# Kernel optimization log

Hardware: AMD Instinct MI355X
Metric: run time of the kernel (lower is better)

The kernel has to match this reference:

```python
import jax, jax.numpy as jnp
import numpy as np

NUM_EMBEDDINGS = 512
EMBEDDING_DIM = 64


def setup_inputs() -> dict:
    key = jax.random.key(0)
    k1, k2 = jax.random.split(key)
    # latent from (identity) encoder, channels-last so view(-1, D) is valid
    z = jax.random.normal(k1, (32, 64, 64, EMBEDDING_DIM), dtype=jnp.float32)
    # codebook init: uniform(-1/K, 1/K) as in the torch module
    scale = 1.0 / NUM_EMBEDDINGS
    codebook = jax.random.uniform(
        k2, (NUM_EMBEDDINGS, EMBEDDING_DIM), dtype=jnp.float32,
        minval=-scale, maxval=scale)
    return {"z": z, "codebook": codebook}


def reference(z, codebook):
    # encoder = identity
    B, H, W, D = z.shape
    zf = z.reshape(-1, D)                                   # [N, D]
    # squared L2 distances: ||z||^2 + ||e||^2 - 2 z.e
    d = (jnp.sum(zf * zf, axis=1, keepdims=True)
         + jnp.sum(codebook * codebook, axis=1)
         - 2.0 * jnp.matmul(zf, codebook.T))                # [N, K]
    idx = jnp.argmin(d, axis=1)                             # [N]
    z_quantized = codebook[idx].reshape(z.shape)            # gather + reshape
    # decoder = identity
    x_recon = z_quantized
    return (x_recon, z_quantized)
```

## Files before the change

### kernel.cpp

```cpp
#include <hip/hip_runtime.h>
#include <math.h>

#define K_CODES 512
#define DIM 64
#define ROWS_PER_BLOCK 128
#define MROWS 128

__device__ __forceinline__ float np_pairwise_sumsq(const float* v) {
#pragma clang fp contract(off)
    float p[DIM];
#pragma unroll
    for (int j = 0; j < DIM; ++j) p[j] = v[j] * v[j];
    float r[8];
#pragma unroll
    for (int a = 0; a < 8; ++a) r[a] = p[a];
#pragma unroll
    for (int i = 8; i < DIM; i += 8) {
#pragma unroll
        for (int a = 0; a < 8; ++a) r[a] = r[a] + p[i + a];
    }
    return ((r[0] + r[1]) + (r[2] + r[3])) + ((r[4] + r[5]) + (r[6] + r[7]));
}

__device__ __forceinline__ float np_dot8acc(const float* zr, const float* ck) {
#pragma clang fp contract(off)
    float a0 = 0.f, a1 = 0.f, a2 = 0.f, a3 = 0.f;
    float a4 = 0.f, a5 = 0.f, a6 = 0.f, a7 = 0.f;
#pragma unroll
    for (int j = 0; j < DIM; j += 8) {
        a0 = fmaf(zr[j + 0], ck[j + 0], a0);
        a1 = fmaf(zr[j + 1], ck[j + 1], a1);
        a2 = fmaf(zr[j + 2], ck[j + 2], a2);
        a3 = fmaf(zr[j + 3], ck[j + 3], a3);
        a4 = fmaf(zr[j + 4], ck[j + 4], a4);
        a5 = fmaf(zr[j + 5], ck[j + 5], a5);
        a6 = fmaf(zr[j + 6], ck[j + 6], a6);
        a7 = fmaf(zr[j + 7], ck[j + 7], a7);
    }
    return ((a0 + a1) + (a2 + a3)) + ((a4 + a5) + (a6 + a7));
}

__global__ __launch_bounds__(256, 4) void vq_argmin_gather(
    const float* __restrict__ z, const float* __restrict__ cb,
    float* __restrict__ out, int n_rows) {
#pragma clang fp contract(off)
    __shared__ float esq_lds[K_CODES];
    __shared__ float red_d[ROWS_PER_BLOCK];
    __shared__ int   red_b[ROWS_PER_BLOCK];
    __shared__ int   best_lds[ROWS_PER_BLOCK];

    const int t = threadIdx.x;
    const int tr  = t & (ROWS_PER_BLOCK - 1);
    const int row = blockIdx.x * ROWS_PER_BLOCK + tr;
    const int k0 = __builtin_amdgcn_readfirstlane((t >> 7) << 8);

    float zr[DIM];
    const float4* zp = (const float4*)(z + (size_t)row * DIM);
#pragma unroll
    for (int j = 0; j < DIM / 4; ++j) {
        float4 v = zp[j];
        zr[4 * j + 0] = v.x; zr[4 * j + 1] = v.y;
        zr[4 * j + 2] = v.z; zr[4 * j + 3] = v.w;
    }
#pragma unroll
    for (int j = 0; j < DIM; ++j) { asm volatile("" : "+v"(zr[j])); }

    for (int c = t; c < K_CODES; c += 256)
        esq_lds[c] = np_pairwise_sumsq(cb + (size_t)c * DIM);
    __syncthreads();

    const float zsq = np_pairwise_sumsq(zr);
    float dmin = INFINITY;
    int best = k0;
    const float* __restrict__ cbase = cb + (size_t)k0 * DIM;
#pragma unroll 2
    for (int kk = 0; kk < K_CODES / 2; ++kk) {
        const float dot = np_dot8acc(zr, cbase + (size_t)kk * DIM);
        const float tkv = zsq + esq_lds[k0 + kk];
        const float m = 2.0f * dot;
        const float d = tkv - m;
        if (d < dmin) { dmin = d; best = k0 + kk; }
    }
    if (t >= ROWS_PER_BLOCK) { red_d[tr] = dmin; red_b[tr] = best; }
    __syncthreads();
    if (t < ROWS_PER_BLOCK) {
        int b = (red_d[tr] < dmin) ? red_b[tr] : best;
        best_lds[tr] = b;
    }
    __syncthreads();

    const float4* cb4 = (const float4*)cb;
    float4* o = (float4*)out;
    const size_t out1_off = (size_t)n_rows * (DIM / 4);
    const size_t grow = (size_t)blockIdx.x * ROWS_PER_BLOCK * (DIM / 4);
#pragma unroll
    for (int i = t; i < ROWS_PER_BLOCK * (DIM / 4); i += 256) {
        const int r = i >> 4;
        const int j = i & 15;
        const float4 v = cb4[(size_t)best_lds[r] * (DIM / 4) + j];
        const size_t g = grow + (size_t)r * (DIM / 4) + j;
        o[g] = v;
        o[g + out1_off] = v;
    }
}

typedef __bf16 bfx8 __attribute__((ext_vector_type(8)));
typedef float  f32x4 __attribute__((ext_vector_type(4)));

#define EPS_GAP 3.0e-5f

__device__ __forceinline__ void split_bf16(float x, unsigned short& h, unsigned short& l) {
    unsigned int xb = __float_as_uint(x);
    unsigned int hb = (xb + 0x8000u) & 0xffff0000u;
    h = (unsigned short)(hb >> 16);
    float lf = x - __uint_as_float(hb);
    l = (unsigned short)((__float_as_uint(lf) + 0x8000u) >> 16);
}

__global__ void vq_prep(const float* __restrict__ cb,
                        unsigned short* __restrict__ wh,
                        unsigned short* __restrict__ wl,
                        float* __restrict__ esq,
                        int* __restrict__ gcnt) {
    const int id = blockIdx.x * 256 + threadIdx.x;
    if (id == 0) gcnt[0] = 0;
    const int l = id & 63;
    const int s = (id >> 6) & 1;
    const int t = id >> 7;
    const int code = t * 16 + (l & 15);
    const int d0 = s * 32 + (l >> 4) * 8;
    const float* p = cb + (size_t)code * DIM + d0;
    float4 v0 = *(const float4*)p;
    float4 v1 = *(const float4*)(p + 4);
    float f[8] = {v0.x, v0.y, v0.z, v0.w, v1.x, v1.y, v1.z, v1.w};
    union { unsigned short u[8]; uint4 q; } H, L;
#pragma unroll
    for (int j = 0; j < 8; ++j) split_bf16(f[j], H.u[j], L.u[j]);
    *(uint4*)(wh + (size_t)id * 8) = H.q;
    *(uint4*)(wl + (size_t)id * 8) = L.q;
    if (id < K_CODES) esq[id] = np_pairwise_sumsq(cb + (size_t)id * DIM);
}

__global__ __launch_bounds__(512)
__attribute__((amdgpu_waves_per_eu(1, 2))) void vq_mfma_main(
    const float* __restrict__ z,
    const unsigned short* __restrict__ wfrag,
    const float* __restrict__ esq_g,
    const float* __restrict__ cb,
    float* __restrict__ out,
    int* __restrict__ gcnt, int* __restrict__ grows,
    int n_rows) {
    __shared__ unsigned short b_lds[K_CODES * DIM * 2];
    __shared__ float esq_lds[K_CODES];
    __shared__ int   best_lds[MROWS];

    const int t = threadIdx.x;
    const int wave = t >> 6;
    const int lane = t & 63;
    const int lg = lane >> 4;
    const int lr = lane & 15;
    const int rb = blockIdx.x * MROWS;
    const int wrb = rb + wave * 16;

    {
        const uint4* src = (const uint4*)wfrag;
        uint4* dst = (uint4*)b_lds;
#pragma unroll
        for (int i = 0; i < 16; ++i) dst[t + i * 512] = src[t + i * 512];
    }
    if (t < K_CODES) esq_lds[t] = esq_g[t];

    bfx8 a_hi[2], a_lo[2];
#pragma unroll
    for (int s = 0; s < 2; ++s) {
        const float* zp = z + (size_t)(wrb + lr) * DIM + s * 32 + lg * 8;
        float4 v0 = *(const float4*)zp;
        float4 v1 = *(const float4*)(zp + 4);
        float f[8] = {v0.x, v0.y, v0.z, v0.w, v1.x, v1.y, v1.z, v1.w};
        union { unsigned short u[8]; bfx8 b; } H, L;
#pragma unroll
        for (int j = 0; j < 8; ++j) split_bf16(f[j], H.u[j], L.u[j]);
        a_hi[s] = H.b;
        a_lo[s] = L.b;
    }
    __syncthreads();

    float b1[4], b2[4];
    int   k1[4];
#pragma unroll
    for (int i = 0; i < 4; ++i) { b1[i] = INFINITY; b2[i] = INFINITY; k1[i] = 0; }

    for (int tt = 0; tt < 32; ++tt) {
        const int s0 = ((tt * 2 + 0) * 64 + lane) * 8;
        const int s1 = ((tt * 2 + 1) * 64 + lane) * 8;
        bfx8 bh0 = *(const bfx8*)(b_lds + s0);
        bfx8 bh1 = *(const bfx8*)(b_lds + s1);
        bfx8 bl0 = *(const bfx8*)(b_lds + 32768 + s0);
        bfx8 bl1 = *(const bfx8*)(b_lds + 32768 + s1);

        f32x4 acc = {0.f, 0.f, 0.f, 0.f};
        acc = __builtin_amdgcn_mfma_f32_16x16x32_bf16(a_hi[0], bh0, acc, 0, 0, 0);
        acc = __builtin_amdgcn_mfma_f32_16x16x32_bf16(a_hi[1], bh1, acc, 0, 0, 0);
        acc = __builtin_amdgcn_mfma_f32_16x16x32_bf16(a_hi[0], bl0, acc, 0, 0, 0);
        acc = __builtin_amdgcn_mfma_f32_16x16x32_bf16(a_hi[1], bl1, acc, 0, 0, 0);
        acc = __builtin_amdgcn_mfma_f32_16x16x32_bf16(a_lo[0], bh0, acc, 0, 0, 0);
        acc = __builtin_amdgcn_mfma_f32_16x16x32_bf16(a_lo[1], bh1, acc, 0, 0, 0);

        const float ev = esq_lds[tt * 16 + lr];
        const int   kk = tt * 16 + lr;
#pragma unroll
        for (int i = 0; i < 4; ++i) {
            float s = fmaf(-2.0f, acc[i], ev);
            b2[i] = fminf(fmaxf(s, b1[i]), b2[i]);
            bool c = s < b1[i];
            b1[i] = c ? s : b1[i];
            k1[i] = c ? kk : k1[i];
        }
    }

#pragma unroll
    for (int m = 1; m <= 8; m <<= 1) {
#pragma unroll
        for (int i = 0; i < 4; ++i) {
            float ob1 = __shfl_xor(b1[i], m);
            int   ok1 = __shfl_xor(k1[i], m);
            float ob2 = __shfl_xor(b2[i], m);
            float nb2 = fminf(fmaxf(b1[i], ob1), fminf(b2[i], ob2));
            bool take = (ob1 < b1[i]) || (ob1 == b1[i] && ok1 < k1[i]);
            b1[i] = take ? ob1 : b1[i];
            k1[i] = take ? ok1 : k1[i];
            b2[i] = nb2;
        }
    }

    if (lr == 0) {
#pragma unroll
        for (int i = 0; i < 4; ++i) {
            const int rl = wave * 16 + lg * 4 + i;
            best_lds[rl] = k1[i];
            if (b2[i] - b1[i] <= EPS_GAP) {
                int p = atomicAdd(gcnt, 1);
                grows[p] = rb + rl;
            }
        }
    }
    __syncthreads();

    const float4* cb4 = (const float4*)cb;
    float4* o = (float4*)out;
    const size_t out1_off = (size_t)n_rows * (DIM / 4);
    const size_t grow = (size_t)blockIdx.x * MROWS * (DIM / 4);
#pragma unroll
    for (int i = t; i < MROWS * (DIM / 4); i += 512) {
        const int r = i >> 4;
        const int j = i & 15;
        const float4 v = cb4[(size_t)best_lds[r] * (DIM / 4) + j];
        const size_t g = grow + (size_t)r * (DIM / 4) + j;
        o[g] = v;
        o[g + out1_off] = v;
    }
}

__global__ __launch_bounds__(256, 1) void vq_fixup(
    const float* __restrict__ z, const float* __restrict__ cb,
    const float* __restrict__ esq_g,
    const int* __restrict__ gcnt, const int* __restrict__ grows,
    float* __restrict__ out, int n_rows) {
#pragma clang fp contract(off)
    const int lane = threadIdx.x & 63;
    const int wid = (blockIdx.x * 256 + threadIdx.x) >> 6;
    const int nf = gcnt[0];

    for (int fi = wid; fi < nf; fi += 1024) {
        const int row = __builtin_amdgcn_readfirstlane(grows[fi]);
        const float* zp = z + (size_t)row * DIM;
        float zs[DIM];
#pragma unroll
        for (int j = 0; j < DIM; ++j) zs[j] = zp[j];

        const float zsq = np_pairwise_sumsq(zs);
        float dmin = INFINITY;
        int bk = lane * 8;
        const float* cbase = cb + (size_t)(lane * 8) * DIM;
#pragma unroll
        for (int c = 0; c < 8; ++c) {
            const float dot = np_dot8acc(zs, cbase + (size_t)c * DIM);
            const float tkv = zsq + esq_g[lane * 8 + c];
            const float m2 = 2.0f * dot;
            const float d = tkv - m2;
            if (d < dmin) { dmin = d; bk = lane * 8 + c; }
        }
#pragma unroll
        for (int m = 1; m <= 32; m <<= 1) {
            float od = __shfl_xor(dmin, m);
            int   ob = __shfl_xor(bk, m);
            bool take = (od < dmin) || (od == dmin && ob < bk);
            dmin = take ? od : dmin;
            bk = take ? ob : bk;
        }
        if (lane < 16) {
            const float4 v = ((const float4*)cb)[(size_t)bk * (DIM / 4) + lane];
            float4* o = (float4*)out;
            const size_t g = (size_t)row * (DIM / 4) + lane;
            o[g] = v;
            o[g + (size_t)n_rows * (DIM / 4)] = v;
        }
    }
}

extern "C" void kernel_launch(void* const* d_in, const int* in_sizes, int n_in,
                              void* d_out, int out_size, void* d_ws, size_t ws_size,
                              hipStream_t stream) {
    const float* z  = (const float*)d_in[0];
    const float* cb = (const float*)d_in[1];
    float* out = (float*)d_out;

    const int n_rows = in_sizes[0] / DIM;

    const size_t frag_elems = (size_t)K_CODES * DIM;
    const size_t WS_NEED = frag_elems * 2 * 2 + K_CODES * 4 + 16 + (size_t)n_rows * 4;
    if (ws_size >= WS_NEED && (n_rows % MROWS) == 0) {
        unsigned short* wh = (unsigned short*)d_ws;
        unsigned short* wl = wh + frag_elems;
        float* esq = (float*)(wl + frag_elems);
        int* gcnt  = (int*)(esq + K_CODES);
        int* grows = gcnt + 4;
        vq_prep<<<dim3(16), dim3(256), 0, stream>>>(cb, wh, wl, esq, gcnt);
        vq_mfma_main<<<dim3(n_rows / MROWS), dim3(512), 0, stream>>>(
            z, wh, esq, cb, out, gcnt, grows, n_rows);
        vq_fixup<<<dim3(256), dim3(256), 0, stream>>>(
            z, cb, esq, gcnt, grows, out, n_rows);
    } else {
        vq_argmin_gather<<<dim3(n_rows / ROWS_PER_BLOCK), dim3(256), 0, stream>>>(
            z, cb, out, n_rows);
    }
}
```

Baseline: 167.6 us.

## Switch to 32x32x16 MFMA tiles and process 512 rows per block

Replaces the 16x16x32 bf16 MFMA tiling with 32x32x16 tiles, so each wave handles 32 rows against 32 codes per step. It also re-lays out the codebook fragments in the prep kernel to match. Each block now covers 512 rows in two sequential groups, amortising the 128KB LDS codebook load over four times as many rows. The aim is fewer LDS reads per FLOP and less per-block staging overhead. The costs are a larger register footprint (16 accumulators plus 16 running best/second-best/index values), more shuffle reduction steps, and only 256 blocks, which may reduce occupancy and tail balance.

```diff
diff --git a/kernel.cpp b/kernel.cpp
--- a/kernel.cpp
+++ b/kernel.cpp
@@ -4,7 +4,8 @@
 #define K_CODES 512
 #define DIM 64
 #define ROWS_PER_BLOCK 128
-#define MROWS 128
+#define BROWS 512
+#define GROUPS 2
 
 __device__ __forceinline__ float np_pairwise_sumsq(const float* v) {
 #pragma clang fp contract(off)
@@ -105,7 +106,7 @@
 }
 
 typedef __bf16 bfx8 __attribute__((ext_vector_type(8)));
-typedef float  f32x4 __attribute__((ext_vector_type(4)));
+typedef float  f32x16 __attribute__((ext_vector_type(16)));
 
 #define EPS_GAP 3.0e-5f
 
@@ -125,10 +126,10 @@
     const int id = blockIdx.x * 256 + threadIdx.x;
     if (id == 0) gcnt[0] = 0;
     const int l = id & 63;
-    const int s = (id >> 6) & 1;
-    const int t = id >> 7;
-    const int code = t * 16 + (l & 15);
-    const int d0 = s * 32 + (l >> 4) * 8;
+    const int kk = (id >> 6) & 3;
+    const int tile = id >> 8;
+    const int code = tile * 32 + (l & 31);
+    const int d0 = kk * 16 + (l >> 5) * 8;
     const float* p = cb + (size_t)code * DIM + d0;
     float4 v0 = *(const float4*)p;
     float4 v1 = *(const float4*)(p + 4);
@@ -152,15 +153,14 @@
     int n_rows) {
     __shared__ unsigned short b_lds[K_CODES * DIM * 2];
     __shared__ float esq_lds[K_CODES];
-    __shared__ int   best_lds[MROWS];
+    __shared__ int   best_lds[BROWS];
 
     const int t = threadIdx.x;
     const int wave = t >> 6;
     const int lane = t & 63;
-    const int lg = lane >> 4;
-    const int lr = lane & 15;
-    const int rb = blockIdx.x * MROWS;
-    const int wrb = rb + wave * 16;
+    const int lc = lane & 31;
+    const int lh = lane >> 5;
+    const int rb = blockIdx.x * BROWS;
 
     {
         const uint4* src = (const uint4*)wfrag;
@@ -169,78 +169,88 @@
         for (int i = 0; i < 16; ++i) dst[t + i * 512] = src[t + i * 512];
     }
     if (t < K_CODES) esq_lds[t] = esq_g[t];
-
-    bfx8 a_hi[2], a_lo[2];
-#pragma unroll
-    for (int s = 0; s < 2; ++s) {
-        const float* zp = z + (size_t)(wrb + lr) * DIM + s * 32 + lg * 8;
-        float4 v0 = *(const float4*)zp;
-        float4 v1 = *(const float4*)(zp + 4);
-        float f[8] = {v0.x, v0.y, v0.z, v0.w, v1.x, v1.y, v1.z, v1.w};
-        union { unsigned short u[8]; bfx8 b; } H, L;
-#pragma unroll
-        for (int j = 0; j < 8; ++j) split_bf16(f[j], H.u[j], L.u[j]);
-        a_hi[s] = H.b;
-        a_lo[s] = L.b;
-    }
-    __syncthreads();
-
-    float b1[4], b2[4];
-    int   k1[4];
-#pragma unroll
-    for (int i = 0; i < 4; ++i) { b1[i] = INFINITY; b2[i] = INFINITY; k1[i] = 0; }
-
-    for (int tt = 0; tt < 32; ++tt) {
-        const int s0 = ((tt * 2 + 0) * 64 + lane) * 8;
-        const int s1 = ((tt * 2 + 1) * 64 + lane) * 8;
-        bfx8 bh0 = *(const bfx8*)(b_lds + s0);
-        bfx8 bh1 = *(const bfx8*)(b_lds + s1);
-        bfx8 bl0 = *(const bfx8*)(b_lds + 32768 + s0);
-        bfx8 bl1 = *(const bfx8*)(b_lds + 32768 + s1);
-
-        f32x4 acc = {0.f, 0.f, 0.f, 0.f};
-        acc = __builtin_amdgcn_mfma_f32_16x16x32_bf16(a_hi[0], bh0, acc, 0, 0, 0);
-        acc = __builtin_amdgcn_mfma_f32_16x16x32_bf16(a_hi[1], bh1, acc, 0, 0, 0);
-        acc = __builtin_amdgcn_mfma_f32_16x16x32_bf16(a_hi[0], bl0, acc, 0, 0, 0);
-        acc = __builtin_amdgcn_mfma_f32_16x16x32_bf16(a_hi[1], bl1, acc, 0, 0, 0);
-        acc = __builtin_amdgcn_mfma_f32_16x16x32_bf16(a_lo[0], bh0, acc, 0, 0, 0);
-        acc = __builtin_amdgcn_mfma_f32_16x16x32_bf16(a_lo[1], bh1, acc, 0, 0, 0);
-
-        const float ev = esq_lds[tt * 16 + lr];
-        const int   kk = tt * 16 + lr;
-#pragma unroll
-        for (int i = 0; i < 4; ++i) {
-            float s = fmaf(-2.0f, acc[i], ev);
-            b2[i] = fminf(fmaxf(s, b1[i]), b2[i]);
-            bool c = s < b1[i];
-            b1[i] = c ? s : b1[i];
-            k1[i] = c ? kk : k1[i];
-        }
-    }
-
-#pragma unroll
-    for (int m = 1; m <= 8; m <<= 1) {
-#pragma unroll
-        for (int i = 0; i < 4; ++i) {
-            float ob1 = __shfl_xor(b1[i], m);
-            int   ok1 = __shfl_xor(k1[i], m);
-            float ob2 = __shfl_xor(b2[i], m);
-            float nb2 = fminf(fmaxf(b1[i], ob1), fminf(b2[i], ob2));
-            bool take = (ob1 < b1[i]) || (ob1 == b1[i] && ok1 < k1[i]);
-            b1[i] = take ? ob1 : b1[i];
-            k1[i] = take ? ok1 : k1[i];
-            b2[i] = nb2;
-        }
-    }
-
-    if (lr == 0) {
-#pragma unroll
-        for (int i = 0; i < 4; ++i) {
-            const int rl = wave * 16 + lg * 4 + i;
-            best_lds[rl] = k1[i];
-            if (b2[i] - b1[i] <= EPS_GAP) {
-                int p = atomicAdd(gcnt, 1);
-                grows[p] = rb + rl;
+    __syncthreads();
+
+#pragma unroll 1
+    for (int g = 0; g < GROUPS; ++g) {
+        const int grb = rb + g * (BROWS / GROUPS) + wave * 32;
+
+        bfx8 a_hi[4], a_lo[4];
+#pragma unroll
+        for (int kk = 0; kk < 4; ++kk) {
+            const float* zp = z + (size_t)(grb + lc) * DIM + kk * 16 + lh * 8;
+            float4 v0 = *(const float4*)zp;
+            float4 v1 = *(const float4*)(zp + 4);
+            float f[8] = {v0.x, v0.y, v0.z, v0.w, v1.x, v1.y, v1.z, v1.w};
+            union { unsigned short u[8]; bfx8 b; } H, L;
+#pragma unroll
+            for (int j = 0; j < 8; ++j) split_bf16(f[j], H.u[j], L.u[j]);
+            a_hi[kk] = H.b;
+            a_lo[kk] = L.b;
+        }
+
+        float b1[16], b2[16];
+        int   k1[16];
+#pragma unroll
+        for (int i = 0; i < 16; ++i) { b1[i] = INFINITY; b2[i] = INFINITY; k1[i] = 0; }
+
+        for (int tt = 0; tt < 16; ++tt) {
+            bfx8 bh[4], bl[4];
+#pragma unroll
+            for (int kk = 0; kk < 4; ++kk) {
+                const int s = ((tt * 4 + kk) * 64 + lane) * 8;
+                bh[kk] = *(const bfx8*)(b_lds + s);
+                bl[kk] = *(const bfx8*)(b_lds + 32768 + s);
+            }
+
+            f32x16 acc = {0.f};
+#pragma unroll
+            for (int kk = 0; kk < 4; ++kk)
+                acc = __builtin_amdgcn_mfma_f32_32x32x16_bf16(a_hi[kk], bh[kk], acc, 0, 0, 0);
+#pragma unroll
+            for (int kk = 0; kk < 4; ++kk)
+                acc = __builtin_amdgcn_mfma_f32_32x32x16_bf16(a_hi[kk], bl[kk], acc, 0, 0, 0);
+#pragma unroll
+            for (int kk = 0; kk < 4; ++kk)
+                acc = __builtin_amdgcn_mfma_f32_32x32x16_bf16(a_lo[kk], bh[kk], acc, 0, 0, 0);
+
+            const float ev = esq_lds[tt * 32 + lc];
+            const int   kc = tt * 32 + lc;
+#pragma unroll
+            for (int r = 0; r < 16; ++r) {
+                float s = fmaf(-2.0f, acc[r], ev);
+                b2[r] = fminf(fmaxf(s, b1[r]), b2[r]);
+                bool c = s < b1[r];
+                b1[r] = c ? s : b1[r];
+                k1[r] = c ? kc : k1[r];
+            }
+        }
+
+#pragma unroll
+        for (int m = 1; m <= 16; m <<= 1) {
+#pragma unroll
+            for (int r = 0; r < 16; ++r) {
+                float ob1 = __shfl_xor(b1[r], m);
+                int   ok1 = __shfl_xor(k1[r], m);
+                float ob2 = __shfl_xor(b2[r], m);
+                float nb2 = fminf(fmaxf(b1[r], ob1), fminf(b2[r], ob2));
+                bool take = (ob1 < b1[r]) || (ob1 == b1[r] && ok1 < k1[r]);
+                b1[r] = take ? ob1 : b1[r];
+                k1[r] = take ? ok1 : k1[r];
+                b2[r] = nb2;
+            }
+        }
+
+        if (lc == 0) {
+#pragma unroll
+            for (int r = 0; r < 16; ++r) {
+                const int rl = g * (BROWS / GROUPS) + wave * 32
+                             + (r & 3) + 8 * (r >> 2) + 4 * lh;
+                best_lds[rl] = k1[r];
+                if (b2[r] - b1[r] <= EPS_GAP) {
+                    int p = atomicAdd(gcnt, 1);
+                    grows[p] = rb + rl;
+                }
             }
         }
     }
@@ -249,9 +259,9 @@
     const float4* cb4 = (const float4*)cb;
     float4* o = (float4*)out;
     const size_t out1_off = (size_t)n_rows * (DIM / 4);
-    const size_t grow = (size_t)blockIdx.x * MROWS * (DIM / 4);
-#pragma unroll
-    for (int i = t; i < MROWS * (DIM / 4); i += 512) {
+    const size_t grow = (size_t)blockIdx.x * BROWS * (DIM / 4);
+#pragma unroll
+    for (int i = t; i < BROWS * (DIM / 4); i += 512) {
         const int r = i >> 4;
         const int j = i & 15;
         const float4 v = cb4[(size_t)best_lds[r] * (DIM / 4) + j];
@@ -319,14 +329,14 @@
 
     const size_t frag_elems = (size_t)K_CODES * DIM;
     const size_t WS_NEED = frag_elems * 2 * 2 + K_CODES * 4 + 16 + (size_t)n_rows * 4;
-    if (ws_size >= WS_NEED && (n_rows % MROWS) == 0) {
+    if (ws_size >= WS_NEED && (n_rows % BROWS) == 0) {
         unsigned short* wh = (unsigned short*)d_ws;
         unsigned short* wl = wh + frag_elems;
         float* esq = (float*)(wl + frag_elems);
         int* gcnt  = (int*)(esq + K_CODES);
         int* grows = gcnt + 4;
         vq_prep<<<dim3(16), dim3(256), 0, stream>>>(cb, wh, wl, esq, gcnt);
-        vq_mfma_main<<<dim3(n_rows / MROWS), dim3(512), 0, stream>>>(
+        vq_mfma_main<<<dim3(n_rows / BROWS), dim3(512), 0, stream>>>(
             z, wh, esq, cb, out, gcnt, grows, n_rows);
         vq_fixup<<<dim3(256), dim3(256), 0, stream>>>(
             z, cb, esq, gcnt, grows, out, n_rows);
```

After: 191.6 us. +14.3%, slower.
